# Kernel tuning notes

Measured on AMD Instinct MI355X. Metric: run time of the kernel, lower is better.

The kernel has to match this reference:

```python
import jax, jax.numpy as jnp
import numpy as np

B, S, D, E, K = 2, 2048, 1024, 8, 2
DFF = 4 * D


def setup_inputs() -> dict:
    key = jax.random.key(0)
    ks = jax.random.split(key, 7)
    scale = 0.02
    return {
        "x": jax.random.normal(ks[0], (B, S, D), dtype=jnp.float32),
        "W1": jax.random.normal(ks[1], (E, D, DFF), dtype=jnp.float32) * scale,
        "b1": jnp.zeros((E, DFF), dtype=jnp.float32),
        "W2": jax.random.normal(ks[2], (E, DFF, D), dtype=jnp.float32) * scale,
        "b2": jnp.zeros((E, D), dtype=jnp.float32),
        "Wg": jax.random.normal(ks[3], (D, E), dtype=jnp.float32) * scale,
        "bg": jnp.zeros((E,), dtype=jnp.float32),
    }


def reference(x, W1, b1, W2, b2, Wg, bg):
    num_experts = W1.shape[0]
    # Gating: top-k logits -> softmax over the k selected experts
    gate_logits = jnp.einsum("bsd,de->bse", x, Wg) + bg          # [B,S,E]
    topk_w, topk_i = jax.lax.top_k(gate_logits, K)               # [B,S,K]
    topk_w = jax.nn.softmax(topk_w, axis=-1)
    # Per-expert combine weight (sum of routed weights, 0 if not routed)
    w = jnp.sum(
        jax.nn.one_hot(topk_i, num_experts, dtype=x.dtype) * topk_w[..., None],
        axis=-2,
    )                                                            # [B,S,E]
    # Faithful to original: every expert runs its full FFN over all tokens,
    # then outputs are masked by routing weights and summed.
    h = jax.nn.gelu(jnp.einsum("bsd,edf->bsef", x, W1) + b1, approximate=False)
    out = jnp.einsum("bsef,efd,bse->bsd", h, W2, w)
    out = out + jnp.einsum("bse,ed->bsd", w, b2)
    return out
```

## Files before the change

kernel.cpp:

```cpp
#include <hip/hip_runtime.h>
#include <math.h>

#define TOK 4096
#define D 1024
#define DFF 4096
#define NE 8
#define CAP 4096
#define YSLOTS 9216
#define NTMAX 72
#define GTOK 16

typedef _Float16 half4v __attribute__((ext_vector_type(4)));
typedef _Float16 half8v __attribute__((ext_vector_type(8)));
typedef float f32x4 __attribute__((ext_vector_type(4)));

#define GLOAD16(gp, lp) __builtin_amdgcn_global_load_lds( \
    (const __attribute__((address_space(1))) void*)(gp),  \
    (__attribute__((address_space(3))) void*)(lp), 16, 0, 0)

__device__ __forceinline__ float fast_gelu(float v) {
    float u = 0.7978845608f * (v + 0.044715f * v * v * v);
    float au = fabsf(u);
    float t = __expf(-2.f * au);
    float th = (1.f - t) / (1.f + t);
    th = u < 0.f ? -th : th;
    return 0.5f * v * (1.f + th);
}

__device__ __forceinline__ void tr_tile(const float* __restrict__ S,
                                        _Float16* __restrict__ T,
                                        int R, int C, int r0, int c0,
                                        char* smem, int tid) {
    float (*tile_t)[129] = (float(*)[129])smem;
    int cl = tid & 63;
    int rl = (tid >> 6) * 32;
#pragma unroll
    for (int k = 0; k < 32; ++k) {
        int r = rl + k;
        tile_t[cl][r] = S[(size_t)(r0 + r) * C + c0 + cl];
    }
    __syncthreads();
    int j = tid & 7;
#pragma unroll
    for (int p = 0; p < 2; ++p) {
        int c = p * 32 + (tid >> 3);
#pragma unroll
        for (int i = 0; i < 2; ++i) {
            int rb = i * 64 + j * 8;
            half8v h;
#pragma unroll
            for (int jj = 0; jj < 8; ++jj) h[jj] = (_Float16)tile_t[c][rb + jj];
            *(half8v*)(T + (size_t)(c0 + c) * R + r0 + rb) = h;
        }
    }
}


__global__ void k_gate_trw1(const float* __restrict__ x, const float* __restrict__ Wg,
                            const float* __restrict__ bg, int* __restrict__ counts,
                            int* __restrict__ tk_e, float* __restrict__ tk_w,
                            int* __restrict__ tk_pos, int* __restrict__ tok_list,
                            _Float16* __restrict__ xh,
                            const float* __restrict__ W1, _Float16* __restrict__ W1t) {
    __shared__ __align__(16) char smem[33024];
    int bid = blockIdx.x;
    int tid = threadIdx.x;
    if (bid >= 256) {
        int t = bid - 256;
        int e = t >> 9, xx = t & 511;
        tr_tile(W1 + (size_t)e * D * DFF, W1t + (size_t)e * DFF * D,
                D, DFF, (xx >> 6) * 128, (xx & 63) * 64, smem, tid);
        return;
    }
    int* s_e = (int*)smem;
    int* s_rank = (int*)(smem + 128);
    int* s_base = (int*)(smem + 256);
    int wid = tid >> 6, lane = tid & 63;
    int tbase = bid * GTOK;

    for (int i = 0; i < 4; ++i) {
        int tl = wid * 4 + i;
        int t = tbase + tl;
        const float* xr = x + (size_t)t * D;
        float a[NE];
#pragma unroll
        for (int e = 0; e < NE; ++e) a[e] = 0.f;
        for (int d = lane; d < D; d += 64) {
            float xv = xr[d];
            const float4 w0 = *(const float4*)(Wg + d * NE);
            const float4 w1 = *(const float4*)(Wg + d * NE + 4);
            a[0] += xv * w0.x; a[1] += xv * w0.y; a[2] += xv * w0.z; a[3] += xv * w0.w;
            a[4] += xv * w1.x; a[5] += xv * w1.y; a[6] += xv * w1.z; a[7] += xv * w1.w;
        }
#pragma unroll
        for (int j = 0; j < 2; ++j) {
            int ch = j * 64 + lane;
            float4 va = *(const float4*)(xr + ch * 8);
            float4 vb = *(const float4*)(xr + ch * 8 + 4);
            half8v h;
            h[0] = (_Float16)va.x; h[1] = (_Float16)va.y; h[2] = (_Float16)va.z; h[3] = (_Float16)va.w;
            h[4] = (_Float16)vb.x; h[5] = (_Float16)vb.y; h[6] = (_Float16)vb.z; h[7] = (_Float16)vb.w;
            *(half8v*)(xh + (size_t)t * D + ch * 8) = h;
        }
#pragma unroll
        for (int m = 1; m < 64; m <<= 1) {
#pragma unroll
            for (int e = 0; e < NE; ++e) a[e] += __shfl_xor(a[e], m, 64);
        }
        if (lane == 0) {
#pragma unroll
            for (int e = 0; e < NE; ++e) a[e] += bg[e];
            int i0 = 0;
#pragma unroll
            for (int e = 1; e < NE; ++e) if (a[e] > a[i0]) i0 = e;
            int i1 = (i0 == 0) ? 1 : 0;
#pragma unroll
            for (int e = 0; e < NE; ++e) if (e != i0 && a[e] > a[i1]) i1 = e;
            float ee = expf(a[i1] - a[i0]);
            float w0 = 1.f / (1.f + ee);
            float w1 = ee / (1.f + ee);
            tk_e[t * 2] = i0; tk_e[t * 2 + 1] = i1;
            tk_w[t * 2] = w0; tk_w[t * 2 + 1] = w1;
            s_e[tl * 2] = i0; s_e[tl * 2 + 1] = i1;
        }
    }
    __syncthreads();
    if (tid < 2 * GTOK) {
        int ei = s_e[tid];
        int r = 0;
#pragma unroll
        for (int j = 0; j < 2 * GTOK; ++j) r += (j < tid && s_e[j] == ei) ? 1 : 0;
        s_rank[tid] = r;
    } else if (tid >= 64 && tid < 64 + NE) {
        int e = tid - 64;
        int cnt = 0;
#pragma unroll
        for (int j = 0; j < 2 * GTOK; ++j) cnt += (s_e[j] == e) ? 1 : 0;
        s_base[e] = cnt ? atomicAdd(&counts[e], cnt) : 0;
    }
    __syncthreads();
    if (tid < 2 * GTOK) {
        int ei = s_e[tid];
        int t = tbase + (tid >> 1);
        int pos = s_base[ei] + s_rank[tid];
        tok_list[ei * CAP + pos] = t;
        tk_pos[t * 2 + (tid & 1)] = pos;
    }
}

__global__ void k_prep(const int* __restrict__ counts, int* __restrict__ offs) {
    int o = 0;
    for (int e = 0; e < NE; ++e) { offs[e] = o; o += (counts[e] + 127) & ~127; }
    offs[NE] = o;
}

__global__ __launch_bounds__(256, 4)
void k_ffn1_trw2(const _Float16* __restrict__ xh, const _Float16* __restrict__ W1t,
                 const float* __restrict__ b1, const int* __restrict__ counts,
                 const int* __restrict__ offs, const int* __restrict__ tok_list,
                 _Float16* __restrict__ H,
                 const float* __restrict__ W2, _Float16* __restrict__ W2t) {
    __shared__ __align__(16) char smem[34816];
    int bid = blockIdx.x;
    int tid = threadIdx.x;
    if (bid >= 2304) {
        int t = bid - 2304;
        int e = t >> 9, xx = t & 511;
        tr_tile(W2 + (size_t)e * DFF * D, W2t + (size_t)e * D * DFF,
                DFF, D, (xx >> 4) * 128, (xx & 15) * 64, smem, tid);
        return;
    }
    int T = bid >> 5;
    if (T * 128 >= offs[NE]) return;
    int e = 0;
#pragma unroll
    for (int k = 1; k < NE; ++k) if (offs[k] <= T * 128) e = k;
    int row0 = T * 128 - offs[e];
    int n_e = counts[e];
    int bx = bid & 31;

    _Float16* As = (_Float16*)smem;
    _Float16* Bs = (_Float16*)(smem + 16384);
    int* s_tok = (int*)(smem + 32768);

    int lane = tid & 63, wid = tid >> 6;
    if (tid < 128) {
        int m = row0 + tid;
        s_tok[tid] = tok_list[e * CAP + (m < n_e ? m : n_e - 1)];
    }
    __syncthreads();

    int srow = lane >> 3, u = lane & 7;
    int wm = (wid >> 1) * 64, wn = (wid & 1) * 64;
    int cl = lane & 15, g = lane >> 4;
    int v8 = u ^ srow;
    int rbase = wid * 32 + srow;

    const _Float16* Abase = W1t + (size_t)e * DFF * D + (size_t)(bx * 128) * D + v8 * 8;
    const _Float16* bsrc[4];
#pragma unroll
    for (int i = 0; i < 4; ++i)
        bsrc[i] = xh + (size_t)s_tok[rbase + i * 8] * D + v8 * 8;

    f32x4 acc[4][4];
#pragma unroll
    for (int i = 0; i < 4; ++i)
#pragma unroll
        for (int j = 0; j < 4; ++j) acc[i][j] = (f32x4)0.f;

    for (int kt = 0; kt < D; kt += 64) {
#pragma unroll
        for (int i = 0; i < 4; ++i)
            GLOAD16(Abase + (size_t)(rbase + i * 8) * D + kt, As + (wid * 4 + i) * 512);
#pragma unroll
        for (int i = 0; i < 4; ++i)
            GLOAD16(bsrc[i] + kt, Bs + (wid * 4 + i) * 512);
        __syncthreads();
#pragma unroll
        for (int ks = 0; ks < 2; ++ks) {
            half8v aF[4], bF[4];
            int vv = ((ks * 4 + g) ^ (cl & 7)) * 8;
#pragma unroll
            for (int fm = 0; fm < 4; ++fm)
                aF[fm] = *(const half8v*)(As + (wm + fm * 16 + cl) * 64 + vv);
#pragma unroll
            for (int fn = 0; fn < 4; ++fn)
                bF[fn] = *(const half8v*)(Bs + (wn + fn * 16 + cl) * 64 + vv);
#pragma unroll
            for (int fm = 0; fm < 4; ++fm)
#pragma unroll
                for (int fn = 0; fn < 4; ++fn)
                    acc[fm][fn] = __builtin_amdgcn_mfma_f32_16x16x32_f16(aF[fm], bF[fn], acc[fm][fn], 0, 0, 0);
        }
        __syncthreads();
    }

    _Float16* Tile = (_Float16*)smem;
#pragma unroll
    for (int fm = 0; fm < 4; ++fm) {
        int featl = wm + fm * 16 + g * 4;
        float4 bv = *(const float4*)(b1 + e * DFF + bx * 128 + featl);
        float bb[4] = {bv.x, bv.y, bv.z, bv.w};
#pragma unroll
        for (int fn = 0; fn < 4; ++fn) {
            int sl = wn + fn * 16 + cl;
            half4v hv;
#pragma unroll
            for (int j = 0; j < 4; ++j) {
                float vv2 = acc[fm][fn][j] + bb[j];
                hv[j] = (_Float16)fast_gelu(vv2);
            }
            *(half4v*)(&Tile[sl * 136 + featl]) = hv;
        }
    }
    __syncthreads();
#pragma unroll
    for (int p = 0; p < 8; ++p) {
        int r = p * 16 + (tid >> 4);
        int c8 = (tid & 15) * 8;
        if (row0 + r < n_e)
            *(half8v*)(H + (size_t)(T * 128 + r) * DFF + bx * 128 + c8) =
                *(const half8v*)(&Tile[r * 136 + c8]);
    }
}

__global__ __launch_bounds__(256, 4)
void k_ffn2(const _Float16* __restrict__ H, const _Float16* __restrict__ W2t,
            const int* __restrict__ counts, const int* __restrict__ offs,
            _Float16* __restrict__ Yh) {
    int wg = blockIdx.x;
    int xcd = wg & 7, j = wg >> 3;
    int bx = j & 7;
    int tl = (j >> 3) % 9;
    int kh = j / 72;
    int T = xcd * 9 + tl;
    if (T * 128 >= offs[NE]) return;
    int e = 0;
#pragma unroll
    for (int k = 1; k < NE; ++k) if (offs[k] <= T * 128) e = k;
    int row0 = T * 128 - offs[e];
    int n_e = counts[e];

    __shared__ __align__(16) char smem[34816];
    _Float16* As = (_Float16*)smem;
    _Float16* Bs = (_Float16*)(smem + 16384);

    int tid = threadIdx.x, lane = tid & 63, wid = tid >> 6;
    int srow = lane >> 3, u = lane & 7;
    int wm = (wid >> 1) * 64, wn = (wid & 1) * 64;
    int cl = lane & 15, g = lane >> 4;
    int v8 = u ^ srow;
    int rbase = wid * 32 + srow;

    const _Float16* Abase = W2t + (size_t)e * D * DFF + (size_t)(bx * 128) * DFF + v8 * 8;
    const _Float16* Bbase = H + (size_t)(T * 128) * DFF + v8 * 8;

    f32x4 acc[4][4];
#pragma unroll
    for (int i = 0; i < 4; ++i)
#pragma unroll
        for (int j2 = 0; j2 < 4; ++j2) acc[i][j2] = (f32x4)0.f;

    int kt0 = kh * 2048, kt1 = kt0 + 2048;
    for (int kt = kt0; kt < kt1; kt += 64) {
#pragma unroll
        for (int i = 0; i < 4; ++i)
            GLOAD16(Abase + (size_t)(rbase + i * 8) * DFF + kt, As + (wid * 4 + i) * 512);
#pragma unroll
        for (int i = 0; i < 4; ++i)
            GLOAD16(Bbase + (size_t)(rbase + i * 8) * DFF + kt, Bs + (wid * 4 + i) * 512);
        __syncthreads();
#pragma unroll
        for (int ks = 0; ks < 2; ++ks) {
            half8v aF[4], bF[4];
            int vv = ((ks * 4 + g) ^ (cl & 7)) * 8;
#pragma unroll
            for (int fm = 0; fm < 4; ++fm)
                aF[fm] = *(const half8v*)(As + (wm + fm * 16 + cl) * 64 + vv);
#pragma unroll
            for (int fn = 0; fn < 4; ++fn)
                bF[fn] = *(const half8v*)(Bs + (wn + fn * 16 + cl) * 64 + vv);
#pragma unroll
            for (int fm = 0; fm < 4; ++fm)
#pragma unroll
                for (int fn = 0; fn < 4; ++fn)
                    acc[fm][fn] = __builtin_amdgcn_mfma_f32_16x16x32_f16(aF[fm], bF[fn], acc[fm][fn], 0, 0, 0);
        }
        __syncthreads();
    }

    _Float16* Tile = (_Float16*)smem;
#pragma unroll
    for (int fm = 0; fm < 4; ++fm) {
        int dl = wm + fm * 16 + g * 4;
#pragma unroll
        for (int fn = 0; fn < 4; ++fn) {
            int sl = wn + fn * 16 + cl;
            half4v hv;
#pragma unroll
            for (int j2 = 0; j2 < 4; ++j2) hv[j2] = (_Float16)acc[fm][fn][j2];
            *(half4v*)(&Tile[sl * 136 + dl]) = hv;
        }
    }
    __syncthreads();
#pragma unroll
    for (int p = 0; p < 8; ++p) {
        int r = p * 16 + (tid >> 4);
        int c8 = (tid & 15) * 8;
        if (row0 + r < n_e)
            *(half8v*)(Yh + ((size_t)kh * YSLOTS + T * 128 + r) * D + bx * 128 + c8) =
                *(const half8v*)(&Tile[r * 136 + c8]);
    }
}

__global__ void k_comb(const int* __restrict__ tk_e, const float* __restrict__ tk_w,
                       const int* __restrict__ tk_pos, const int* __restrict__ offs,
                       const _Float16* __restrict__ Yh, const float* __restrict__ b2,
                       float* __restrict__ out) {
    int idx = blockIdx.x * 256 + threadIdx.x;
    int t = idx >> 8;
    int d = (idx & 255) * 4;
    int e0 = tk_e[2 * t], e1 = tk_e[2 * t + 1];
    float w0 = tk_w[2 * t], w1 = tk_w[2 * t + 1];
    size_t s0 = offs[e0] + tk_pos[2 * t];
    size_t s1 = offs[e1] + tk_pos[2 * t + 1];
    half4v y00 = *(const half4v*)(Yh + s0 * D + d);
    half4v y01 = *(const half4v*)(Yh + ((size_t)YSLOTS + s0) * D + d);
    half4v y10 = *(const half4v*)(Yh + s1 * D + d);
    half4v y11 = *(const half4v*)(Yh + ((size_t)YSLOTS + s1) * D + d);
    float4 b20 = *(const float4*)(b2 + e0 * D + d);
    float4 b21 = *(const float4*)(b2 + e1 * D + d);
    float4 r;
    r.x = w0 * ((float)y00[0] + (float)y01[0] + b20.x) + w1 * ((float)y10[0] + (float)y11[0] + b21.x);
    r.y = w0 * ((float)y00[1] + (float)y01[1] + b20.y) + w1 * ((float)y10[1] + (float)y11[1] + b21.y);
    r.z = w0 * ((float)y00[2] + (float)y01[2] + b20.z) + w1 * ((float)y10[2] + (float)y11[2] + b21.z);
    r.w = w0 * ((float)y00[3] + (float)y01[3] + b20.w) + w1 * ((float)y10[3] + (float)y11[3] + b21.w);
    *(float4*)(out + (size_t)t * D + d) = r;
}

extern "C" void kernel_launch(void* const* d_in, const int* in_sizes, int n_in,
                              void* d_out, int out_size, void* d_ws, size_t ws_size,
                              hipStream_t stream) {
    const float* x  = (const float*)d_in[0];
    const float* W1 = (const float*)d_in[1];
    const float* b1 = (const float*)d_in[2];
    const float* W2 = (const float*)d_in[3];
    const float* b2 = (const float*)d_in[4];
    const float* Wg = (const float*)d_in[5];
    const float* bg = (const float*)d_in[6];
    float* out = (float*)d_out;

    char* ws = (char*)d_ws;
    int*   counts   = (int*)(ws);
    int*   offs     = (int*)(ws + 64);
    int*   tk_e     = (int*)(ws + 256);
    float* tk_w     = (float*)(ws + 33024);
    int*   tk_pos   = (int*)(ws + 65792);
    int*   tok_list = (int*)(ws + 98560);
    _Float16* xh    = (_Float16*)(ws + (1ull << 20));
    _Float16* W1t   = (_Float16*)(ws + (10ull << 20));
    _Float16* Yh    = (_Float16*)(ws + (10ull << 20));
    _Float16* W2t   = (_Float16*)(ws + (74ull << 20));
    _Float16* H     = (_Float16*)(ws + (138ull << 20));

    hipMemsetAsync(counts, 0, 64, stream);
    k_gate_trw1<<<256 + 4096, 256, 0, stream>>>(x, Wg, bg, counts, tk_e, tk_w, tk_pos,
                                                tok_list, xh, W1, W1t);
    k_prep<<<1, 1, 0, stream>>>(counts, offs);
    k_ffn1_trw2<<<2304 + 4096, 256, 0, stream>>>(xh, W1t, b1, counts, offs, tok_list,
                                                 H, W2, W2t);
    k_ffn2<<<8 * 144, 256, 0, stream>>>(H, W2t, counts, offs, Yh);
    k_comb<<<(TOK * D / 4) / 256, 256, 0, stream>>>(tk_e, tk_w, tk_pos, offs, Yh, b2, out);
}
```

Measured before the change: 297.6 us.

## Double-buffer GEMM K-loop with async LDS loads and drop offset-prep kernel

Result: slower. 314.0 us (+5.5%).

```diff
diff --git a/kernel.cpp b/kernel.cpp
--- a/kernel.cpp
+++ b/kernel.cpp
@@ -25,6 +25,12 @@
     float th = (1.f - t) / (1.f + t);
     th = u < 0.f ? -th : th;
     return 0.5f * v * (1.f + th);
+}
+
+__device__ __forceinline__ void mk_offs(const int* __restrict__ counts, int* offE) {
+    offE[0] = 0;
+#pragma unroll
+    for (int k = 0; k < NE; ++k) offE[k + 1] = offE[k] + ((counts[k] + 127) & ~127);
 }
 
 __device__ __forceinline__ void tr_tile(const float* __restrict__ S,
@@ -148,17 +154,10 @@
     }
 }
 
-__global__ void k_prep(const int* __restrict__ counts, int* __restrict__ offs) {
-    int o = 0;
-    for (int e = 0; e < NE; ++e) { offs[e] = o; o += (counts[e] + 127) & ~127; }
-    offs[NE] = o;
-}
-
 __global__ __launch_bounds__(256, 4)
 void k_ffn1_trw2(const _Float16* __restrict__ xh, const _Float16* __restrict__ W1t,
                  const float* __restrict__ b1, const int* __restrict__ counts,
-                 const int* __restrict__ offs, const int* __restrict__ tok_list,
-                 _Float16* __restrict__ H,
+                 const int* __restrict__ tok_list, _Float16* __restrict__ H,
                  const float* __restrict__ W2, _Float16* __restrict__ W2t) {
     __shared__ __align__(16) char smem[34816];
     int bid = blockIdx.x;
@@ -170,17 +169,18 @@
                 DFF, D, (xx >> 4) * 128, (xx & 15) * 64, smem, tid);
         return;
     }
+    int offE[NE + 1];
+    mk_offs(counts, offE);
     int T = bid >> 5;
-    if (T * 128 >= offs[NE]) return;
+    if (T * 128 >= offE[NE]) return;
     int e = 0;
 #pragma unroll
-    for (int k = 1; k < NE; ++k) if (offs[k] <= T * 128) e = k;
-    int row0 = T * 128 - offs[e];
+    for (int k = 1; k < NE; ++k) if (offE[k] <= T * 128) e = k;
+    int row0 = T * 128 - offE[e];
     int n_e = counts[e];
     int bx = bid & 31;
 
-    _Float16* As = (_Float16*)smem;
-    _Float16* Bs = (_Float16*)(smem + 16384);
+    _Float16* SH = (_Float16*)smem;
     int* s_tok = (int*)(smem + 32768);
 
     int lane = tid & 63, wid = tid >> 6;
@@ -190,50 +190,57 @@
     }
     __syncthreads();
 
-    int srow = lane >> 3, u = lane & 7;
+    int l4 = lane >> 2, u = lane & 3;
+    int gu8 = (u ^ (l4 & 3)) * 8;
     int wm = (wid >> 1) * 64, wn = (wid & 1) * 64;
     int cl = lane & 15, g = lane >> 4;
-    int v8 = u ^ srow;
-    int rbase = wid * 32 + srow;
-
-    const _Float16* Abase = W1t + (size_t)e * DFF * D + (size_t)(bx * 128) * D + v8 * 8;
-    const _Float16* bsrc[4];
+
+    int rA0 = wid * 16 + l4;
+    const _Float16* W1e = W1t + (size_t)e * DFF * D;
+    const _Float16* Asrc0 = W1e + (size_t)(bx * 128 + rA0) * D + gu8;
+    const _Float16* Asrc1 = Asrc0 + (size_t)64 * D;
+    const _Float16* Bsrc0 = xh + (size_t)s_tok[rA0] * D + gu8;
+    const _Float16* Bsrc1 = xh + (size_t)s_tok[rA0 + 64] * D + gu8;
+    __syncthreads();
+
+    int ldsA = wid * 512;
+    int ldsB = 4096 + wid * 512;
+
+#define STG1(c, KT) { \
+    GLOAD16(Asrc0 + (KT), SH + (c) * 8192 + ldsA); \
+    GLOAD16(Asrc1 + (KT), SH + (c) * 8192 + ldsA + 2048); \
+    GLOAD16(Bsrc0 + (KT), SH + (c) * 8192 + ldsB); \
+    GLOAD16(Bsrc1 + (KT), SH + (c) * 8192 + ldsB + 2048); }
+
+    f32x4 acc[4][4];
 #pragma unroll
     for (int i = 0; i < 4; ++i)
-        bsrc[i] = xh + (size_t)s_tok[rbase + i * 8] * D + v8 * 8;
-
-    f32x4 acc[4][4];
-#pragma unroll
-    for (int i = 0; i < 4; ++i)
 #pragma unroll
         for (int j = 0; j < 4; ++j) acc[i][j] = (f32x4)0.f;
 
-    for (int kt = 0; kt < D; kt += 64) {
-#pragma unroll
-        for (int i = 0; i < 4; ++i)
-            GLOAD16(Abase + (size_t)(rbase + i * 8) * D + kt, As + (wid * 4 + i) * 512);
-#pragma unroll
-        for (int i = 0; i < 4; ++i)
-            GLOAD16(bsrc[i] + kt, Bs + (wid * 4 + i) * 512);
+    int vv = (g ^ (cl & 3)) * 8;
+    STG1(0, 0)
+    __syncthreads();
+    for (int t = 0; t < 32; ++t) {
+        int c = t & 1;
+        if (t + 1 < 32) STG1((t + 1) & 1, (t + 1) * 32)
+        const _Float16* Ab = SH + c * 8192;
+        const _Float16* Bb = SH + c * 8192 + 4096;
+        half8v aF[4], bF[4];
+#pragma unroll
+        for (int fm = 0; fm < 4; ++fm)
+            aF[fm] = *(const half8v*)(Ab + (wm + fm * 16 + cl) * 32 + vv);
+#pragma unroll
+        for (int fn = 0; fn < 4; ++fn)
+            bF[fn] = *(const half8v*)(Bb + (wn + fn * 16 + cl) * 32 + vv);
+#pragma unroll
+        for (int fm = 0; fm < 4; ++fm)
+#pragma unroll
+            for (int fn = 0; fn < 4; ++fn)
+                acc[fm][fn] = __builtin_amdgcn_mfma_f32_16x16x32_f16(aF[fm], bF[fn], acc[fm][fn], 0, 0, 0);
         __syncthreads();
-#pragma unroll
-        for (int ks = 0; ks < 2; ++ks) {
-            half8v aF[4], bF[4];
-            int vv = ((ks * 4 + g) ^ (cl & 7)) * 8;
-#pragma unroll
-            for (int fm = 0; fm < 4; ++fm)
-                aF[fm] = *(const half8v*)(As + (wm + fm * 16 + cl) * 64 + vv);
-#pragma unroll
-            for (int fn = 0; fn < 4; ++fn)
-                bF[fn] = *(const half8v*)(Bs + (wn + fn * 16 + cl) * 64 + vv);
-#pragma unroll
-            for (int fm = 0; fm < 4; ++fm)
-#pragma unroll
-                for (int fn = 0; fn < 4; ++fn)
-                    acc[fm][fn] = __builtin_amdgcn_mfma_f32_16x16x32_f16(aF[fm], bF[fn], acc[fm][fn], 0, 0, 0);
-        }
-        __syncthreads();
-    }
+    }
+#undef STG1
 
     _Float16* Tile = (_Float16*)smem;
 #pragma unroll
@@ -266,34 +273,46 @@
 
 __global__ __launch_bounds__(256, 4)
 void k_ffn2(const _Float16* __restrict__ H, const _Float16* __restrict__ W2t,
-            const int* __restrict__ counts, const int* __restrict__ offs,
-            _Float16* __restrict__ Yh) {
+            const int* __restrict__ counts, _Float16* __restrict__ Yh) {
     int wg = blockIdx.x;
     int xcd = wg & 7, j = wg >> 3;
     int bx = j & 7;
     int tl = (j >> 3) % 9;
     int kh = j / 72;
     int T = xcd * 9 + tl;
-    if (T * 128 >= offs[NE]) return;
+    int offE[NE + 1];
+    mk_offs(counts, offE);
+    if (T * 128 >= offE[NE]) return;
     int e = 0;
 #pragma unroll
-    for (int k = 1; k < NE; ++k) if (offs[k] <= T * 128) e = k;
-    int row0 = T * 128 - offs[e];
+    for (int k = 1; k < NE; ++k) if (offE[k] <= T * 128) e = k;
+    int row0 = T * 128 - offE[e];
     int n_e = counts[e];
 
     __shared__ __align__(16) char smem[34816];
-    _Float16* As = (_Float16*)smem;
-    _Float16* Bs = (_Float16*)(smem + 16384);
+    _Float16* SH = (_Float16*)smem;
 
     int tid = threadIdx.x, lane = tid & 63, wid = tid >> 6;
-    int srow = lane >> 3, u = lane & 7;
+    int l4 = lane >> 2, u = lane & 3;
+    int gu8 = (u ^ (l4 & 3)) * 8;
     int wm = (wid >> 1) * 64, wn = (wid & 1) * 64;
     int cl = lane & 15, g = lane >> 4;
-    int v8 = u ^ srow;
-    int rbase = wid * 32 + srow;
-
-    const _Float16* Abase = W2t + (size_t)e * D * DFF + (size_t)(bx * 128) * DFF + v8 * 8;
-    const _Float16* Bbase = H + (size_t)(T * 128) * DFF + v8 * 8;
+
+    int rA0 = wid * 16 + l4;
+    const _Float16* W2e = W2t + (size_t)e * D * DFF;
+    const _Float16* Asrc0 = W2e + (size_t)(bx * 128 + rA0) * DFF + gu8;
+    const _Float16* Asrc1 = Asrc0 + (size_t)64 * DFF;
+    const _Float16* Bsrc0 = H + (size_t)(T * 128 + rA0) * DFF + gu8;
+    const _Float16* Bsrc1 = Bsrc0 + (size_t)64 * DFF;
+
+    int ldsA = wid * 512;
+    int ldsB = 4096 + wid * 512;
+
+#define STG2(c, KT) { \
+    GLOAD16(Asrc0 + (KT), SH + (c) * 8192 + ldsA); \
+    GLOAD16(Asrc1 + (KT), SH + (c) * 8192 + ldsA + 2048); \
+    GLOAD16(Bsrc0 + (KT), SH + (c) * 8192 + ldsB); \
+    GLOAD16(Bsrc1 + (KT), SH + (c) * 8192 + ldsB + 2048); }
 
     f32x4 acc[4][4];
 #pragma unroll
@@ -301,33 +320,30 @@
 #pragma unroll
         for (int j2 = 0; j2 < 4; ++j2) acc[i][j2] = (f32x4)0.f;
 
-    int kt0 = kh * 2048, kt1 = kt0 + 2048;
-    for (int kt = kt0; kt < kt1; kt += 64) {
-#pragma unroll
-        for (int i = 0; i < 4; ++i)
-            GLOAD16(Abase + (size_t)(rbase + i * 8) * DFF + kt, As + (wid * 4 + i) * 512);
-#pragma unroll
-        for (int i = 0; i < 4; ++i)
-            GLOAD16(Bbase + (size_t)(rbase + i * 8) * DFF + kt, Bs + (wid * 4 + i) * 512);
+    int vv = (g ^ (cl & 3)) * 8;
+    int kt0 = kh * 2048;
+    STG2(0, kt0)
+    __syncthreads();
+    for (int t = 0; t < 64; ++t) {
+        int c = t & 1;
+        if (t + 1 < 64) STG2((t + 1) & 1, kt0 + (t + 1) * 32)
+        const _Float16* Ab = SH + c * 8192;
+        const _Float16* Bb = SH + c * 8192 + 4096;
+        half8v aF[4], bF[4];
+#pragma unroll
+        for (int fm = 0; fm < 4; ++fm)
+            aF[fm] = *(const half8v*)(Ab + (wm + fm * 16 + cl) * 32 + vv);
+#pragma unroll
+        for (int fn = 0; fn < 4; ++fn)
+            bF[fn] = *(const half8v*)(Bb + (wn + fn * 16 + cl) * 32 + vv);
+#pragma unroll
+        for (int fm = 0; fm < 4; ++fm)
+#pragma unroll
+            for (int fn = 0; fn < 4; ++fn)
+                acc[fm][fn] = __builtin_amdgcn_mfma_f32_16x16x32_f16(aF[fm], bF[fn], acc[fm][fn], 0, 0, 0);
         __syncthreads();
-#pragma unroll
-        for (int ks = 0; ks < 2; ++ks) {
-            half8v aF[4], bF[4];
-            int vv = ((ks * 4 + g) ^ (cl & 7)) * 8;
-#pragma unroll
-            for (int fm = 0; fm < 4; ++fm)
-                aF[fm] = *(const half8v*)(As + (wm + fm * 16 + cl) * 64 + vv);
-#pragma unroll
-            for (int fn = 0; fn < 4; ++fn)
-                bF[fn] = *(const half8v*)(Bs + (wn + fn * 16 + cl) * 64 + vv);
-#pragma unroll
-            for (int fm = 0; fm < 4; ++fm)
-#pragma unroll
-                for (int fn = 0; fn < 4; ++fn)
-                    acc[fm][fn] = __builtin_amdgcn_mfma_f32_16x16x32_f16(aF[fm], bF[fn], acc[fm][fn], 0, 0, 0);
-        }
-        __syncthreads();
-    }
+    }
+#undef STG2
 
     _Float16* Tile = (_Float16*)smem;
 #pragma unroll
@@ -354,16 +370,18 @@
 }
 
 __global__ void k_comb(const int* __restrict__ tk_e, const float* __restrict__ tk_w,
-                       const int* __restrict__ tk_pos, const int* __restrict__ offs,
+                       const int* __restrict__ tk_pos, const int* __restrict__ counts,
                        const _Float16* __restrict__ Yh, const float* __restrict__ b2,
                        float* __restrict__ out) {
     int idx = blockIdx.x * 256 + threadIdx.x;
     int t = idx >> 8;
     int d = (idx & 255) * 4;
+    int offE[NE + 1];
+    mk_offs(counts, offE);
     int e0 = tk_e[2 * t], e1 = tk_e[2 * t + 1];
     float w0 = tk_w[2 * t], w1 = tk_w[2 * t + 1];
-    size_t s0 = offs[e0] + tk_pos[2 * t];
-    size_t s1 = offs[e1] + tk_pos[2 * t + 1];
+    size_t s0 = offE[e0] + tk_pos[2 * t];
+    size_t s1 = offE[e1] + tk_pos[2 * t + 1];
     half4v y00 = *(const half4v*)(Yh + s0 * D + d);
     half4v y01 = *(const half4v*)(Yh + ((size_t)YSLOTS + s0) * D + d);
     half4v y10 = *(const half4v*)(Yh + s1 * D + d);
@@ -392,7 +410,6 @@
 
     char* ws = (char*)d_ws;
     int*   counts   = (int*)(ws);
-    int*   offs     = (int*)(ws + 64);
     int*   tk_e     = (int*)(ws + 256);
     float* tk_w     = (float*)(ws + 33024);
     int*   tk_pos   = (int*)(ws + 65792);
@@ -406,9 +423,8 @@
     hipMemsetAsync(counts, 0, 64, stream);
     k_gate_trw1<<<256 + 4096, 256, 0, stream>>>(x, Wg, bg, counts, tk_e, tk_w, tk_pos,
                                                 tok_list, xh, W1, W1t);
-    k_prep<<<1, 1, 0, stream>>>(counts, offs);
-    k_ffn1_trw2<<<2304 + 4096, 256, 0, stream>>>(xh, W1t, b1, counts, offs, tok_list,
+    k_ffn1_trw2<<<2304 + 4096, 256, 0, stream>>>(xh, W1t, b1, counts, tok_list,
                                                  H, W2, W2t);
-    k_ffn2<<<8 * 144, 256, 0, stream>>>(H, W2t, counts, offs, Yh);
-    k_comb<<<(TOK * D / 4) / 256, 256, 0, stream>>>(tk_e, tk_w, tk_pos, offs, Yh, b2, out);
-}
+    k_ffn2<<<8 * 144, 256, 0, stream>>>(H, W2t, counts, Yh);
+    k_comb<<<(TOK * D / 4) / 256, 256, 0, stream>>>(tk_e, tk_w, tk_pos, counts, Yh, b2, out);
+}
```

## Drop split-K in FFN2 and inline expert offset computation, removing prep kernel

Applied to the files above, without the earlier changes.

Measured after the change: 301.4 us. About the same (+1.3%).

```diff
diff --git a/kernel.cpp b/kernel.cpp
--- a/kernel.cpp
+++ b/kernel.cpp
@@ -7,7 +7,6 @@
 #define NE 8
 #define CAP 4096
 #define YSLOTS 9216
-#define NTMAX 72
 #define GTOK 16
 
 typedef _Float16 half4v __attribute__((ext_vector_type(4)));
@@ -25,6 +24,12 @@
     float th = (1.f - t) / (1.f + t);
     th = u < 0.f ? -th : th;
     return 0.5f * v * (1.f + th);
+}
+
+__device__ __forceinline__ void mk_offs(const int* __restrict__ counts, int* offE) {
+    offE[0] = 0;
+#pragma unroll
+    for (int k = 0; k < NE; ++k) offE[k + 1] = offE[k] + ((counts[k] + 127) & ~127);
 }
 
 __device__ __forceinline__ void tr_tile(const float* __restrict__ S,
@@ -148,17 +153,10 @@
     }
 }
 
-__global__ void k_prep(const int* __restrict__ counts, int* __restrict__ offs) {
-    int o = 0;
-    for (int e = 0; e < NE; ++e) { offs[e] = o; o += (counts[e] + 127) & ~127; }
-    offs[NE] = o;
-}
-
 __global__ __launch_bounds__(256, 4)
 void k_ffn1_trw2(const _Float16* __restrict__ xh, const _Float16* __restrict__ W1t,
                  const float* __restrict__ b1, const int* __restrict__ counts,
-                 const int* __restrict__ offs, const int* __restrict__ tok_list,
-                 _Float16* __restrict__ H,
+                 const int* __restrict__ tok_list, _Float16* __restrict__ H,
                  const float* __restrict__ W2, _Float16* __restrict__ W2t) {
     __shared__ __align__(16) char smem[34816];
     int bid = blockIdx.x;
@@ -170,12 +168,14 @@
                 DFF, D, (xx >> 4) * 128, (xx & 15) * 64, smem, tid);
         return;
     }
+    int offE[NE + 1];
+    mk_offs(counts, offE);
     int T = bid >> 5;
-    if (T * 128 >= offs[NE]) return;
+    if (T * 128 >= offE[NE]) return;
     int e = 0;
 #pragma unroll
-    for (int k = 1; k < NE; ++k) if (offs[k] <= T * 128) e = k;
-    int row0 = T * 128 - offs[e];
+    for (int k = 1; k < NE; ++k) if (offE[k] <= T * 128) e = k;
+    int row0 = T * 128 - offE[e];
     int n_e = counts[e];
     int bx = bid & 31;
 
@@ -266,19 +266,19 @@
 
 __global__ __launch_bounds__(256, 4)
 void k_ffn2(const _Float16* __restrict__ H, const _Float16* __restrict__ W2t,
-            const int* __restrict__ counts, const int* __restrict__ offs,
-            _Float16* __restrict__ Yh) {
+            const int* __restrict__ counts, _Float16* __restrict__ Yh) {
     int wg = blockIdx.x;
     int xcd = wg & 7, j = wg >> 3;
     int bx = j & 7;
-    int tl = (j >> 3) % 9;
-    int kh = j / 72;
+    int tl = j >> 3;
     int T = xcd * 9 + tl;
-    if (T * 128 >= offs[NE]) return;
+    int offE[NE + 1];
+    mk_offs(counts, offE);
+    if (T * 128 >= offE[NE]) return;
     int e = 0;
 #pragma unroll
-    for (int k = 1; k < NE; ++k) if (offs[k] <= T * 128) e = k;
-    int row0 = T * 128 - offs[e];
+    for (int k = 1; k < NE; ++k) if (offE[k] <= T * 128) e = k;
+    int row0 = T * 128 - offE[e];
     int n_e = counts[e];
 
     __shared__ __align__(16) char smem[34816];
@@ -301,8 +301,7 @@
 #pragma unroll
         for (int j2 = 0; j2 < 4; ++j2) acc[i][j2] = (f32x4)0.f;
 
-    int kt0 = kh * 2048, kt1 = kt0 + 2048;
-    for (int kt = kt0; kt < kt1; kt += 64) {
+    for (int kt = 0; kt < DFF; kt += 64) {
 #pragma unroll
         for (int i = 0; i < 4; ++i)
             GLOAD16(Abase + (size_t)(rbase + i * 8) * DFF + kt, As + (wid * 4 + i) * 512);
@@ -348,33 +347,33 @@
         int r = p * 16 + (tid >> 4);
         int c8 = (tid & 15) * 8;
         if (row0 + r < n_e)
-            *(half8v*)(Yh + ((size_t)kh * YSLOTS + T * 128 + r) * D + bx * 128 + c8) =
+            *(half8v*)(Yh + (size_t)(T * 128 + r) * D + bx * 128 + c8) =
                 *(const half8v*)(&Tile[r * 136 + c8]);
     }
 }
 
 __global__ void k_comb(const int* __restrict__ tk_e, const float* __restrict__ tk_w,
-                       const int* __restrict__ tk_pos, const int* __restrict__ offs,
+                       const int* __restrict__ tk_pos, const int* __restrict__ counts,
                        const _Float16* __restrict__ Yh, const float* __restrict__ b2,
                        float* __restrict__ out) {
     int idx = blockIdx.x * 256 + threadIdx.x;
     int t = idx >> 8;
     int d = (idx & 255) * 4;
+    int offE[NE + 1];
+    mk_offs(counts, offE);
     int e0 = tk_e[2 * t], e1 = tk_e[2 * t + 1];
     float w0 = tk_w[2 * t], w1 = tk_w[2 * t + 1];
-    size_t s0 = offs[e0] + tk_pos[2 * t];
-    size_t s1 = offs[e1] + tk_pos[2 * t + 1];
-    half4v y00 = *(const half4v*)(Yh + s0 * D + d);
-    half4v y01 = *(const half4v*)(Yh + ((size_t)YSLOTS + s0) * D + d);
-    half4v y10 = *(const half4v*)(Yh + s1 * D + d);
-    half4v y11 = *(const half4v*)(Yh + ((size_t)YSLOTS + s1) * D + d);
+    size_t s0 = offE[e0] + tk_pos[2 * t];
+    size_t s1 = offE[e1] + tk_pos[2 * t + 1];
+    half4v y0 = *(const half4v*)(Yh + s0 * D + d);
+    half4v y1 = *(const half4v*)(Yh + s1 * D + d);
     float4 b20 = *(const float4*)(b2 + e0 * D + d);
     float4 b21 = *(const float4*)(b2 + e1 * D + d);
     float4 r;
-    r.x = w0 * ((float)y00[0] + (float)y01[0] + b20.x) + w1 * ((float)y10[0] + (float)y11[0] + b21.x);
-    r.y = w0 * ((float)y00[1] + (float)y01[1] + b20.y) + w1 * ((float)y10[1] + (float)y11[1] + b21.y);
-    r.z = w0 * ((float)y00[2] + (float)y01[2] + b20.z) + w1 * ((float)y10[2] + (float)y11[2] + b21.z);
-    r.w = w0 * ((float)y00[3] + (float)y01[3] + b20.w) + w1 * ((float)y10[3] + (float)y11[3] + b21.w);
+    r.x = w0 * ((float)y0[0] + b20.x) + w1 * ((float)y1[0] + b21.x);
+    r.y = w0 * ((float)y0[1] + b20.y) + w1 * ((float)y1[1] + b21.y);
+    r.z = w0 * ((float)y0[2] + b20.z) + w1 * ((float)y1[2] + b21.z);
+    r.w = w0 * ((float)y0[3] + b20.w) + w1 * ((float)y1[3] + b21.w);
     *(float4*)(out + (size_t)t * D + d) = r;
 }
 
@@ -392,7 +391,6 @@
 
     char* ws = (char*)d_ws;
     int*   counts   = (int*)(ws);
-    int*   offs     = (int*)(ws + 64);
     int*   tk_e     = (int*)(ws + 256);
     float* tk_w     = (float*)(ws + 33024);
     int*   tk_pos   = (int*)(ws + 65792);
@@ -406,9 +404,8 @@
     hipMemsetAsync(counts, 0, 64, stream);
     k_gate_trw1<<<256 + 4096, 256, 0, stream>>>(x, Wg, bg, counts, tk_e, tk_w, tk_pos,
                                                 tok_list, xh, W1, W1t);
-    k_prep<<<1, 1, 0, stream>>>(counts, offs);
-    k_ffn1_trw2<<<2304 + 4096, 256, 0, stream>>>(xh, W1t, b1, counts, offs, tok_list,
+    k_ffn1_trw2<<<2304 + 4096, 256, 0, stream>>>(xh, W1t, b1, counts, tok_list,
                                                  H, W2, W2t);
-    k_ffn2<<<8 * 144, 256, 0, stream>>>(H, W2t, counts, offs, Yh);
-    k_comb<<<(TOK * D / 4) / 256, 256, 0, stream>>>(tk_e, tk_w, tk_pos, offs, Yh, b2, out);
-}
+    k_ffn2<<<8 * 72, 256, 0, stream>>>(H, W2t, counts, Yh);
+    k_comb<<<(TOK * D / 4) / 256, 256, 0, stream>>>(tk_e, tk_w, tk_pos, counts, Yh, b2, out);
+}
```
